# Optimization experiments

Hardware: AMD Instinct MI355X
Metric: run time of the kernel (lower is better)

## Reference

```python
import jax, jax.numpy as jnp
import numpy as np

PERTURBATION_SCALE = 0.01

def setup_inputs() -> dict:
    key = jax.random.key(0)
    k1, k2, k3 = jax.random.split(key, 3)
    theta = jax.random.normal(k1, (256, 512), dtype=jnp.float32)
    basis_eval = jax.random.normal(k2, (100000, 512), dtype=jnp.float32)
    noise = jax.random.normal(k3, (256, 512), dtype=jnp.float32)
    return {"theta": theta, "basis_eval": basis_eval, "noise": noise}

def reference(theta, basis_eval, noise):
    # phi: [N, K] functional evaluations
    phi_raw = basis_eval @ theta.T
    phi_perturbed = basis_eval @ (theta + noise * PERTURBATION_SCALE).T
    # sign-crossings between consecutive evaluation points: [N-1, K]
    crossings = (phi_raw[:-1] * phi_raw[1:] < 0).astype(theta.dtype)
    crossings_p = (phi_perturbed[:-1] * phi_perturbed[1:] < 0).astype(theta.dtype)
    persistence = crossings * crossings_p  # [N-1, K]
    # fused pairwise shared-persistence: Gram matrix [K, K]
    gram = persistence.T @ persistence
    K = theta.shape[0]
    iu, ju = jnp.triu_indices(K, k=1)  # row-major i<j == itertools.combinations order
    return gram[iu, ju]  # [K*(K-1)/2]
```

## Files before the change

### kernel.cpp

```cpp
#include <hip/hip_runtime.h>
#include <hip/hip_bf16.h>
#include <stdint.h>

#define KDIM    256
#define NWORDS  1564
#define NW      1563
#define GEMM_GRID 1564

typedef float  f32x4  __attribute__((ext_vector_type(4)));
typedef __bf16 bf16x8 __attribute__((ext_vector_type(8)));

__device__ __forceinline__ void gl_lds16(const void* g, void* l) {
    __builtin_amdgcn_global_load_lds(
        (const __attribute__((address_space(1))) unsigned int*)g,
        (__attribute__((address_space(3))) unsigned int*)l, 16, 0, 0);
}

__global__ void build_w(const float* __restrict__ theta,
                        const float* __restrict__ noise,
                        __bf16* __restrict__ W) {
    int idx = blockIdx.x * 256 + threadIdx.x;
    int j = idx >> 9;
    int d = idx & 511;
    float v;
    if (j < KDIM) v = theta[j * 512 + d];
    else          v = theta[(j - KDIM) * 512 + d] + 0.01f * noise[(j - KDIM) * 512 + d];
    W[idx] = (__bf16)v;
}

__global__ void __launch_bounds__(512, 4)
gemm_signs(const float* __restrict__ basis,
           const __bf16* __restrict__ W,
           uint64_t* __restrict__ sbits) {
    __shared__ char smem[49152];

    const int tid    = threadIdx.x;
    const int lane   = tid & 63;
    const int wave   = tid >> 6;
    const int wr     = wave >> 2;
    const int wc     = wave & 3;
    const int lane16 = lane & 15;
    const int lgrp   = lane >> 4;

    const int orig = blockIdx.x;
    const int xcd  = orig & 7;
    const int wgid = (xcd < 4 ? xcd * 196 : 784 + (xcd - 4) * 195) + (orig >> 3);
    const int bn   = wgid & 1;
    const int bm   = wgid >> 1;

    const int ar = tid >> 2;
    const int ah = tid & 3;
    int arg = bm * 128 + ar; if (arg > 99999) arg = 99999;
    const float* abase_g = basis + (size_t)arg * 512 + ah * 8;
    const int awofs = ar * 64 + ((ah ^ (ar & 3)) << 4);

    auto stage_B = [&](int t) {
        char* bbase = smem + 16384 + ((t & 1) << 14);
        #pragma unroll
        for (int i = 0; i < 2; ++i) {
            int c = wave * 32 + i * 16 + (lane >> 2);
            int g = lane & 3;
            const __bf16* src = W + (size_t)(bn * 256 + c) * 512 + t * 32
                                  + ((g ^ ((c >> 1) & 3)) << 3);
            gl_lds16(src, bbase + (wave * 32 + i * 16) * 64);
        }
    };

    f32x4  acc[4][4] = {};
    float4 ra[2][2];

    ra[0][0] = *(const float4*)(abase_g);
    ra[0][1] = *(const float4*)(abase_g + 4);
    ra[1][0] = *(const float4*)(abase_g + 32);
    ra[1][1] = *(const float4*)(abase_g + 36);
    stage_B(0);
    asm volatile("s_waitcnt vmcnt(4)" ::: "memory");
    {
        bf16x8 a8;
        a8[0] = (__bf16)ra[0][0].x; a8[1] = (__bf16)ra[0][0].y;
        a8[2] = (__bf16)ra[0][0].z; a8[3] = (__bf16)ra[0][0].w;
        a8[4] = (__bf16)ra[0][1].x; a8[5] = (__bf16)ra[0][1].y;
        a8[6] = (__bf16)ra[0][1].z; a8[7] = (__bf16)ra[0][1].w;
        *(bf16x8*)(smem + awofs) = a8;
    }

    #pragma unroll
    for (int t = 0; t < 16; ++t) {
        if (t < 14) {
            ra[t & 1][0] = *(const float4*)(abase_g + (t + 2) * 32);
            ra[t & 1][1] = *(const float4*)(abase_g + (t + 2) * 32 + 4);
        }
        if (t < 15) stage_B(t + 1);

        if      (t < 14) asm volatile("s_waitcnt vmcnt(4)\ns_barrier" ::: "memory");
        else if (t == 14) asm volatile("s_waitcnt vmcnt(2)\ns_barrier" ::: "memory");
        else              asm volatile("s_waitcnt vmcnt(0)\ns_barrier" ::: "memory");

        const char* ab = smem + ((t & 1) << 13);
        const char* bb = smem + 16384 + ((t & 1) << 14);

        bf16x8 bf[4];
        #pragma unroll
        for (int n = 0; n < 4; ++n) {
            int cc = wc * 64 + n * 16 + lane16;
            int gb = lgrp ^ ((cc >> 1) & 3);
            bf[n] = *(const bf16x8*)(bb + cc * 64 + gb * 16);
        }
        bf16x8 af[4];
        #pragma unroll
        for (int m = 0; m < 4; ++m) {
            int rr = wr * 64 + m * 16 + lane16;
            af[m] = *(const bf16x8*)(ab + rr * 64 + ((lgrp ^ (rr & 3)) << 4));
        }

        __builtin_amdgcn_s_setprio(1);
        #pragma unroll
        for (int m = 0; m < 4; ++m)
            #pragma unroll
            for (int n = 0; n < 4; ++n)
                acc[m][n] = __builtin_amdgcn_mfma_f32_16x16x32_bf16(
                    af[m], bf[n], acc[m][n], 0, 0, 0);
        __builtin_amdgcn_s_setprio(0);

        if (t < 15) {
            bf16x8 a8;
            a8[0] = (__bf16)ra[(t + 1) & 1][0].x; a8[1] = (__bf16)ra[(t + 1) & 1][0].y;
            a8[2] = (__bf16)ra[(t + 1) & 1][0].z; a8[3] = (__bf16)ra[(t + 1) & 1][0].w;
            a8[4] = (__bf16)ra[(t + 1) & 1][1].x; a8[5] = (__bf16)ra[(t + 1) & 1][1].y;
            a8[6] = (__bf16)ra[(t + 1) & 1][1].z; a8[7] = (__bf16)ra[(t + 1) & 1][1].w;
            *(bf16x8*)(smem + (((t + 1) & 1) << 13) + awofs) = a8;
        }

        asm volatile("s_waitcnt lgkmcnt(0)\ns_barrier" ::: "memory");
    }

    unsigned char* sb = (unsigned char*)smem;
    #pragma unroll
    for (int m = 0; m < 4; ++m) {
        #pragma unroll
        for (int n = 0; n < 4; ++n) {
            int cc = wc * 64 + n * 16 + lane16;
            int rb = wr * 64 + m * 16 + lgrp * 4;
            uint32_t pk = 0;
            #pragma unroll
            for (int r = 0; r < 4; ++r)
                pk |= (acc[m][n][r] < 0.0f ? 1u : 0u) << (8 * r);
            *(uint32_t*)&sb[cc * 136 + rb] = pk;
        }
    }
    asm volatile("s_waitcnt lgkmcnt(0)\ns_barrier" ::: "memory");

    {
        const int col = tid & 255;
        const int wh  = tid >> 8;
        const unsigned char* src = &sb[col * 136 + wh * 64];
        uint64_t wbits = 0;
        #pragma unroll
        for (int k = 0; k < 16; ++k) {
            uint32_t q  = *(const uint32_t*)&src[4 * k];
            uint32_t p4 = ((q & 0x01010101u) * 0x10204080u) >> 28;
            wbits |= (uint64_t)p4 << (4 * k);
        }
        sbits[(size_t)(bm * 2 + wh) * 512 + bn * 256 + col] = wbits;
    }
}

__global__ void crossing_masks(const uint64_t* __restrict__ sbits,
                               uint64_t* __restrict__ maskT) {
    const int w = blockIdx.x;
    const int j = threadIdx.x;
    uint64_t s0r = sbits[(size_t)w * 512 + j];
    uint64_t s0p = sbits[(size_t)w * 512 + 256 + j];
    uint64_t s1r = sbits[(size_t)(w + 1) * 512 + j];
    uint64_t s1p = sbits[(size_t)(w + 1) * 512 + 256 + j];
    uint64_t cr = s0r ^ ((s0r >> 1) | (s1r << 63));
    uint64_t cp = s0p ^ ((s0p >> 1) | (s1p << 63));
    uint64_t m = cr & cp;
    if (w == NW - 1) m &= 0x7FFFFFFFull;
    maskT[(size_t)w * 256 + j] = m;
}

__global__ void zero_out(float* __restrict__ out) {
    int i = blockIdx.x * 256 + threadIdx.x;
    if (i < 32640) out[i] = 0.0f;
}

__global__ void pair_popcount(const uint64_t* __restrict__ maskT,
                              float* __restrict__ out) {
    const int i = blockIdx.x;
    const int c = blockIdx.y;
    const int j = threadIdx.x;
    if (j <= i) return;
    int w0 = c * 196;
    int w1 = w0 + 196; if (w1 > NW) w1 = NW;
    uint32_t sum = 0;
    #pragma unroll 4
    for (int w = w0; w < w1; ++w) {
        uint64_t mi = maskT[(size_t)w * 256 + i];
        uint64_t mj = maskT[(size_t)w * 256 + j];
        sum += (uint32_t)__popcll(mi & mj);
    }
    const size_t idx = (size_t)i * (2 * KDIM - i - 1) / 2 + (size_t)(j - i - 1);
    atomicAdd(&out[idx], (float)sum);
}

extern "C" void kernel_launch(void* const* d_in, const int* in_sizes, int n_in,
                              void* d_out, int out_size, void* d_ws, size_t ws_size,
                              hipStream_t stream) {
    const float* theta = (const float*)d_in[0];
    const float* basis = (const float*)d_in[1];
    const float* noise = (const float*)d_in[2];
    float* out = (float*)d_out;

    char* ws = (char*)d_ws;
    __bf16*   W     = (__bf16*)ws;
    uint64_t* sbits = (uint64_t*)(ws + 524288);
    uint64_t* maskT = (uint64_t*)(ws + 524288 + (size_t)NWORDS * 512 * 8);

    hipLaunchKernelGGL(build_w,        dim3(1024),     dim3(256), 0, stream, theta, noise, W);
    hipLaunchKernelGGL(gemm_signs,     dim3(GEMM_GRID),dim3(512), 0, stream, basis, W, sbits);
    hipLaunchKernelGGL(crossing_masks, dim3(NW),       dim3(256), 0, stream, sbits, maskT);
    hipLaunchKernelGGL(zero_out,       dim3(128),      dim3(256), 0, stream, out);
    hipLaunchKernelGGL(pair_popcount,  dim3(KDIM, 8),  dim3(256), 0, stream, maskT, out);
}
```

Measured before the change: 127.9 us.

## Split sign GEMM into two kernels with different tile shapes for tail balance

The sign-bit GEMM becomes two kernels. The original 128x256-tile kernel now covers only the first half of the rows (782 blocks). A new 256-thread kernel covers the remaining rows with per-wave 64x64 tiles, each wave working independently without block barriers, using 1568 blocks. The aim is better load balance and fewer idle compute units in the tail of a grid that does not divide evenly across the CUs. The cost is an extra launch and a second kernel whose small per-wave tiles reuse less data.

Result: slower. 155.5 us (+21.5%).

```diff
diff --git a/kernel.cpp b/kernel.cpp
--- a/kernel.cpp
+++ b/kernel.cpp
@@ -5,10 +5,10 @@
 #define KDIM    256
 #define NWORDS  1564
 #define NW      1563
-#define GEMM_GRID 1564
 
 typedef float  f32x4  __attribute__((ext_vector_type(4)));
 typedef __bf16 bf16x8 __attribute__((ext_vector_type(8)));
+typedef __bf16 bf16x4 __attribute__((ext_vector_type(4)));
 
 __device__ __forceinline__ void gl_lds16(const void* g, void* l) {
     __builtin_amdgcn_global_load_lds(
@@ -29,9 +29,9 @@
 }
 
 __global__ void __launch_bounds__(512, 4)
-gemm_signs(const float* __restrict__ basis,
-           const __bf16* __restrict__ W,
-           uint64_t* __restrict__ sbits) {
+gemm_signs_a(const float* __restrict__ basis,
+             const __bf16* __restrict__ W,
+             uint64_t* __restrict__ sbits) {
     __shared__ char smem[49152];
 
     const int tid    = threadIdx.x;
@@ -44,13 +44,13 @@
 
     const int orig = blockIdx.x;
     const int xcd  = orig & 7;
-    const int wgid = (xcd < 4 ? xcd * 196 : 784 + (xcd - 4) * 195) + (orig >> 3);
+    const int wgid = (xcd < 6 ? xcd * 98 : 588 + (xcd - 6) * 97) + (orig >> 3);
     const int bn   = wgid & 1;
     const int bm   = wgid >> 1;
 
     const int ar = tid >> 2;
     const int ah = tid & 3;
-    int arg = bm * 128 + ar; if (arg > 99999) arg = 99999;
+    int arg = bm * 128 + ar;
     const float* abase_g = basis + (size_t)arg * 512 + ah * 8;
     const int awofs = ar * 64 + ((ah ^ (ar & 3)) << 4);
 
@@ -86,6 +86,7 @@
 
     #pragma unroll
     for (int t = 0; t < 16; ++t) {
+        const int q = (t + 1) & 1;
         if (t < 14) {
             ra[t & 1][0] = *(const float4*)(abase_g + (t + 2) * 32);
             ra[t & 1][1] = *(const float4*)(abase_g + (t + 2) * 32 + 4);
@@ -128,9 +129,8 @@
             a8[2] = (__bf16)ra[(t + 1) & 1][0].z; a8[3] = (__bf16)ra[(t + 1) & 1][0].w;
             a8[4] = (__bf16)ra[(t + 1) & 1][1].x; a8[5] = (__bf16)ra[(t + 1) & 1][1].y;
             a8[6] = (__bf16)ra[(t + 1) & 1][1].z; a8[7] = (__bf16)ra[(t + 1) & 1][1].w;
-            *(bf16x8*)(smem + (((t + 1) & 1) << 13) + awofs) = a8;
-        }
-
+            *(bf16x8*)(smem + (q << 13) + awofs) = a8;
+        }
         asm volatile("s_waitcnt lgkmcnt(0)\ns_barrier" ::: "memory");
     }
 
@@ -149,7 +149,6 @@
         }
     }
     asm volatile("s_waitcnt lgkmcnt(0)\ns_barrier" ::: "memory");
-
     {
         const int col = tid & 255;
         const int wh  = tid >> 8;
@@ -157,11 +156,144 @@
         uint64_t wbits = 0;
         #pragma unroll
         for (int k = 0; k < 16; ++k) {
-            uint32_t q  = *(const uint32_t*)&src[4 * k];
-            uint32_t p4 = ((q & 0x01010101u) * 0x10204080u) >> 28;
+            uint32_t qv = *(const uint32_t*)&src[4 * k];
+            uint32_t p4 = ((qv & 0x01010101u) * 0x10204080u) >> 28;
             wbits |= (uint64_t)p4 << (4 * k);
         }
         sbits[(size_t)(bm * 2 + wh) * 512 + bn * 256 + col] = wbits;
+    }
+}
+
+__global__ void __launch_bounds__(256, 3)
+gemm_signs_b(const float* __restrict__ basis,
+             const __bf16* __restrict__ W,
+             uint64_t* __restrict__ sbits) {
+    __shared__ char smem[32768];
+
+    const int tid    = threadIdx.x;
+    const int lane   = tid & 63;
+    const int wave   = tid >> 6;
+    const int lane16 = lane & 15;
+    const int lgrp   = lane >> 4;
+
+    const int orig = blockIdx.x;
+    const int lid  = (orig & 7) * 196 + (orig >> 3);
+    const int bn   = lid & 7;
+    const int bm   = lid >> 3;
+
+    char* aw = smem + wave * 8192;
+    char* bw = aw + 4096;
+    const int rowbase = 50048 + bm * 256 + wave * 64;
+    const int arl = lane >> 3;
+    const int agk = lane & 7;
+
+    auto stage_B = [&](int t) {
+        #pragma unroll
+        for (int i = 0; i < 4; ++i) {
+            int c = i * 16 + (lane >> 2);
+            int g = lane & 3;
+            const __bf16* src = W + (size_t)(bn * 64 + c) * 512 + t * 32
+                                  + ((g ^ ((c >> 1) & 3)) << 3);
+            gl_lds16(src, bw + i * 1024);
+        }
+    };
+    float4 ra[8];
+    auto load_A = [&](int t) {
+        #pragma unroll
+        for (int i = 0; i < 8; ++i) {
+            int r = rowbase + arl + 8 * i;
+            if (r > 99999) r = 99999;
+            ra[i] = *(const float4*)(basis + (size_t)r * 512 + t * 32 + agk * 4);
+        }
+    };
+    auto write_A = [&]() {
+        #pragma unroll
+        for (int i = 0; i < 8; ++i) {
+            int rl = arl + 8 * i;
+            bf16x4 v;
+            v[0] = (__bf16)ra[i].x; v[1] = (__bf16)ra[i].y;
+            v[2] = (__bf16)ra[i].z; v[3] = (__bf16)ra[i].w;
+            *(bf16x4*)(aw + rl * 64 + (((agk >> 1) ^ (rl & 3)) << 4)
+                       + ((agk & 1) << 3)) = v;
+        }
+    };
+
+    f32x4 acc[4][4] = {};
+
+    load_A(0);
+    stage_B(0);
+    asm volatile("s_waitcnt vmcnt(4)" ::: "memory");
+    write_A();
+
+    #pragma unroll
+    for (int t = 0; t < 16; ++t) {
+        asm volatile("s_waitcnt vmcnt(0) lgkmcnt(0)" ::: "memory");
+        __builtin_amdgcn_sched_barrier(0);
+
+        bf16x8 af[4], bf[4];
+        #pragma unroll
+        for (int m = 0; m < 4; ++m) {
+            int rr = m * 16 + lane16;
+            af[m] = *(const bf16x8*)(aw + rr * 64 + ((lgrp ^ (rr & 3)) << 4));
+        }
+        #pragma unroll
+        for (int n = 0; n < 4; ++n) {
+            int cc = n * 16 + lane16;
+            bf[n] = *(const bf16x8*)(bw + cc * 64 + ((lgrp ^ ((cc >> 1) & 3)) << 4));
+        }
+        asm volatile("s_waitcnt lgkmcnt(0)" ::: "memory");
+        __builtin_amdgcn_sched_barrier(0);
+
+        if (t < 15) { load_A(t + 1); stage_B(t + 1); }
+        __builtin_amdgcn_sched_barrier(0);
+
+        __builtin_amdgcn_s_setprio(1);
+        #pragma unroll
+        for (int m = 0; m < 4; ++m)
+            #pragma unroll
+            for (int n = 0; n < 4; ++n)
+                acc[m][n] = __builtin_amdgcn_mfma_f32_16x16x32_bf16(
+                    af[m], bf[n], acc[m][n], 0, 0, 0);
+        __builtin_amdgcn_s_setprio(0);
+
+        if (t < 15) {
+            asm volatile("s_waitcnt vmcnt(4)" ::: "memory");
+            __builtin_amdgcn_sched_barrier(0);
+            write_A();
+        }
+    }
+
+    asm volatile("s_waitcnt lgkmcnt(0)" ::: "memory");
+    __syncthreads();
+    unsigned char* sb = (unsigned char*)smem;
+    #pragma unroll
+    for (int m = 0; m < 4; ++m) {
+        #pragma unroll
+        for (int n = 0; n < 4; ++n) {
+            int cc = n * 16 + lane16;
+            int rb = wave * 64 + m * 16 + lgrp * 4;
+            uint32_t pk = 0;
+            #pragma unroll
+            for (int r = 0; r < 4; ++r)
+                pk |= (acc[m][n][r] < 0.0f ? 1u : 0u) << (8 * r);
+            *(uint32_t*)&sb[cc * 264 + rb] = pk;
+        }
+    }
+    __syncthreads();
+    {
+        const int col = tid & 63;
+        const int wh  = tid >> 6;
+        const unsigned char* src = &sb[col * 264 + wh * 64];
+        uint64_t wbits = 0;
+        #pragma unroll
+        for (int k = 0; k < 16; ++k) {
+            uint32_t qv = *(const uint32_t*)&src[4 * k];
+            uint32_t p4 = ((qv & 0x01010101u) * 0x10204080u) >> 28;
+            wbits |= (uint64_t)p4 << (4 * k);
+        }
+        int word = 782 + bm * 4 + wh;
+        if (word < NWORDS)
+            sbits[(size_t)word * 512 + bn * 64 + col] = wbits;
     }
 }
 
@@ -217,9 +349,10 @@
     uint64_t* sbits = (uint64_t*)(ws + 524288);
     uint64_t* maskT = (uint64_t*)(ws + 524288 + (size_t)NWORDS * 512 * 8);
 
-    hipLaunchKernelGGL(build_w,        dim3(1024),     dim3(256), 0, stream, theta, noise, W);
-    hipLaunchKernelGGL(gemm_signs,     dim3(GEMM_GRID),dim3(512), 0, stream, basis, W, sbits);
-    hipLaunchKernelGGL(crossing_masks, dim3(NW),       dim3(256), 0, stream, sbits, maskT);
-    hipLaunchKernelGGL(zero_out,       dim3(128),      dim3(256), 0, stream, out);
-    hipLaunchKernelGGL(pair_popcount,  dim3(KDIM, 8),  dim3(256), 0, stream, maskT, out);
-}
+    hipLaunchKernelGGL(build_w,        dim3(1024),    dim3(256), 0, stream, theta, noise, W);
+    hipLaunchKernelGGL(gemm_signs_a,   dim3(782),     dim3(512), 0, stream, basis, W, sbits);
+    hipLaunchKernelGGL(gemm_signs_b,   dim3(1568),    dim3(256), 0, stream, basis, W, sbits);
+    hipLaunchKernelGGL(crossing_masks, dim3(NW),      dim3(256), 0, stream, sbits, maskT);
+    hipLaunchKernelGGL(zero_out,       dim3(128),     dim3(256), 0, stream, out);
+    hipLaunchKernelGGL(pair_popcount,  dim3(KDIM, 8), dim3(256), 0, stream, maskT, out);
+}
```

## Pre-tile and swizzle W per k-step and restructure GEMM barrier pipeline

Applied to the files above, without the earlier changes.

build_w now writes W in a k-tile-major, pre-swizzled layout, so each wave's B-panel stage becomes two contiguous 16-byte global-to-LDS loads per lane instead of scattered strided loads. The main loop moves its barrier ahead of issuing the next B stage, waits on LDS reads before the MFMAs behind a sched_barrier, and drops the trailing per-iteration barrier. Together these aim to cut global load inefficiency and synchronisation per k-step. The cost is serialising LDS reads against the MFMAs, and buffer reuse now depends on subtle barrier ordering.

Result: faster. 122.3 us (-4.4%).

```diff
diff --git a/kernel.cpp b/kernel.cpp
--- a/kernel.cpp
+++ b/kernel.cpp
@@ -18,19 +18,23 @@
 
 __global__ void build_w(const float* __restrict__ theta,
                         const float* __restrict__ noise,
-                        __bf16* __restrict__ W) {
+                        __bf16* __restrict__ Wt) {
     int idx = blockIdx.x * 256 + threadIdx.x;
     int j = idx >> 9;
     int d = idx & 511;
     float v;
     if (j < KDIM) v = theta[j * 512 + d];
     else          v = theta[(j - KDIM) * 512 + d] + 0.01f * noise[(j - KDIM) * 512 + d];
-    W[idx] = (__bf16)v;
+    int t  = d >> 5;
+    int g  = (d >> 3) & 3;
+    int e  = d & 7;
+    int gs = g ^ ((j >> 1) & 3);
+    Wt[(((t << 9) + j) << 5) + (gs << 3) + e] = (__bf16)v;
 }
 
 __global__ void __launch_bounds__(512, 4)
 gemm_signs(const float* __restrict__ basis,
-           const __bf16* __restrict__ W,
+           const __bf16* __restrict__ Wt,
            uint64_t* __restrict__ sbits) {
     __shared__ char smem[49152];
 
@@ -54,20 +58,25 @@
     const float* abase_g = basis + (size_t)arg * 512 + ah * 8;
     const int awofs = ar * 64 + ((ah ^ (ar & 3)) << 4);
 
+    const char* bpanel = (const char*)Wt + ((size_t)bn * 256 << 6) + wave * 2048 + lane * 16;
     auto stage_B = [&](int t) {
-        char* bbase = smem + 16384 + ((t & 1) << 14);
-        #pragma unroll
-        for (int i = 0; i < 2; ++i) {
-            int c = wave * 32 + i * 16 + (lane >> 2);
-            int g = lane & 3;
-            const __bf16* src = W + (size_t)(bn * 256 + c) * 512 + t * 32
-                                  + ((g ^ ((c >> 1) & 3)) << 3);
-            gl_lds16(src, bbase + (wave * 32 + i * 16) * 64);
-        }
+        char* bdst = smem + 16384 + ((t & 1) << 14) + wave * 2048;
+        const char* src = bpanel + ((size_t)t << 15);
+        gl_lds16(src,        bdst);
+        gl_lds16(src + 1024, bdst + 1024);
     };
 
     f32x4  acc[4][4] = {};
     float4 ra[2][2];
+
+    auto cvt_write_A = [&](int slot, int q) {
+        bf16x8 a8;
+        a8[0] = (__bf16)ra[slot][0].x; a8[1] = (__bf16)ra[slot][0].y;
+        a8[2] = (__bf16)ra[slot][0].z; a8[3] = (__bf16)ra[slot][0].w;
+        a8[4] = (__bf16)ra[slot][1].x; a8[5] = (__bf16)ra[slot][1].y;
+        a8[6] = (__bf16)ra[slot][1].z; a8[7] = (__bf16)ra[slot][1].w;
+        *(bf16x8*)(smem + (q << 13) + awofs) = a8;
+    };
 
     ra[0][0] = *(const float4*)(abase_g);
     ra[0][1] = *(const float4*)(abase_g + 4);
@@ -75,14 +84,8 @@
     ra[1][1] = *(const float4*)(abase_g + 36);
     stage_B(0);
     asm volatile("s_waitcnt vmcnt(4)" ::: "memory");
-    {
-        bf16x8 a8;
-        a8[0] = (__bf16)ra[0][0].x; a8[1] = (__bf16)ra[0][0].y;
-        a8[2] = (__bf16)ra[0][0].z; a8[3] = (__bf16)ra[0][0].w;
-        a8[4] = (__bf16)ra[0][1].x; a8[5] = (__bf16)ra[0][1].y;
-        a8[6] = (__bf16)ra[0][1].z; a8[7] = (__bf16)ra[0][1].w;
-        *(bf16x8*)(smem + awofs) = a8;
-    }
+    cvt_write_A(0, 0);
+    asm volatile("s_waitcnt lgkmcnt(0)" ::: "memory");
 
     #pragma unroll
     for (int t = 0; t < 16; ++t) {
@@ -90,11 +93,11 @@
             ra[t & 1][0] = *(const float4*)(abase_g + (t + 2) * 32);
             ra[t & 1][1] = *(const float4*)(abase_g + (t + 2) * 32 + 4);
         }
+
+        if (t < 14) asm volatile("s_waitcnt vmcnt(2)\ns_barrier" ::: "memory");
+        else        asm volatile("s_waitcnt vmcnt(0)\ns_barrier" ::: "memory");
+
         if (t < 15) stage_B(t + 1);
-
-        if      (t < 14) asm volatile("s_waitcnt vmcnt(4)\ns_barrier" ::: "memory");
-        else if (t == 14) asm volatile("s_waitcnt vmcnt(2)\ns_barrier" ::: "memory");
-        else              asm volatile("s_waitcnt vmcnt(0)\ns_barrier" ::: "memory");
 
         const char* ab = smem + ((t & 1) << 13);
         const char* bb = smem + 16384 + ((t & 1) << 14);
@@ -103,8 +106,7 @@
         #pragma unroll
         for (int n = 0; n < 4; ++n) {
             int cc = wc * 64 + n * 16 + lane16;
-            int gb = lgrp ^ ((cc >> 1) & 3);
-            bf[n] = *(const bf16x8*)(bb + cc * 64 + gb * 16);
+            bf[n] = *(const bf16x8*)(bb + cc * 64 + ((lgrp ^ ((cc >> 1) & 3)) << 4));
         }
         bf16x8 af[4];
         #pragma unroll
@@ -112,6 +114,8 @@
             int rr = wr * 64 + m * 16 + lane16;
             af[m] = *(const bf16x8*)(ab + rr * 64 + ((lgrp ^ (rr & 3)) << 4));
         }
+        asm volatile("s_waitcnt lgkmcnt(0)" ::: "memory");
+        __builtin_amdgcn_sched_barrier(0);
 
         __builtin_amdgcn_s_setprio(1);
         #pragma unroll
@@ -123,17 +127,12 @@
         __builtin_amdgcn_s_setprio(0);
 
         if (t < 15) {
-            bf16x8 a8;
-            a8[0] = (__bf16)ra[(t + 1) & 1][0].x; a8[1] = (__bf16)ra[(t + 1) & 1][0].y;
-            a8[2] = (__bf16)ra[(t + 1) & 1][0].z; a8[3] = (__bf16)ra[(t + 1) & 1][0].w;
-            a8[4] = (__bf16)ra[(t + 1) & 1][1].x; a8[5] = (__bf16)ra[(t + 1) & 1][1].y;
-            a8[6] = (__bf16)ra[(t + 1) & 1][1].z; a8[7] = (__bf16)ra[(t + 1) & 1][1].w;
-            *(bf16x8*)(smem + (((t + 1) & 1) << 13) + awofs) = a8;
-        }
-
-        asm volatile("s_waitcnt lgkmcnt(0)\ns_barrier" ::: "memory");
-    }
-
+            cvt_write_A((t + 1) & 1, (t + 1) & 1);
+            asm volatile("s_waitcnt lgkmcnt(0)" ::: "memory");
+        }
+    }
+
+    asm volatile("s_barrier" ::: "memory");
     unsigned char* sb = (unsigned char*)smem;
     #pragma unroll
     for (int m = 0; m < 4; ++m) {
@@ -157,8 +156,8 @@
         uint64_t wbits = 0;
         #pragma unroll
         for (int k = 0; k < 16; ++k) {
-            uint32_t q  = *(const uint32_t*)&src[4 * k];
-            uint32_t p4 = ((q & 0x01010101u) * 0x10204080u) >> 28;
+            uint32_t qv = *(const uint32_t*)&src[4 * k];
+            uint32_t p4 = ((qv & 0x01010101u) * 0x10204080u) >> 28;
             wbits |= (uint64_t)p4 << (4 * k);
         }
         sbits[(size_t)(bm * 2 + wh) * 512 + bn * 256 + col] = wbits;
@@ -213,12 +212,12 @@
     float* out = (float*)d_out;
 
     char* ws = (char*)d_ws;
-    __bf16*   W     = (__bf16*)ws;
+    __bf16*   Wt    = (__bf16*)ws;
     uint64_t* sbits = (uint64_t*)(ws + 524288);
     uint64_t* maskT = (uint64_t*)(ws + 524288 + (size_t)NWORDS * 512 * 8);
 
-    hipLaunchKernelGGL(build_w,        dim3(1024),     dim3(256), 0, stream, theta, noise, W);
-    hipLaunchKernelGGL(gemm_signs,     dim3(GEMM_GRID),dim3(512), 0, stream, basis, W, sbits);
+    hipLaunchKernelGGL(build_w,        dim3(1024),     dim3(256), 0, stream, theta, noise, Wt);
+    hipLaunchKernelGGL(gemm_signs,     dim3(GEMM_GRID),dim3(512), 0, stream, basis, Wt, sbits);
     hipLaunchKernelGGL(crossing_masks, dim3(NW),       dim3(256), 0, stream, sbits, maskT);
     hipLaunchKernelGGL(zero_out,       dim3(128),      dim3(256), 0, stream, out);
     hipLaunchKernelGGL(pair_popcount,  dim3(KDIM, 8),  dim3(256), 0, stream, maskT, out);
```
